# Kernel tuning notes

Hardware: AMD Instinct MI355X
Metric: run time of the kernel (lower is better)

## Reference

```python
import jax, jax.numpy as jnp
import numpy as np

B, S, H = 32, 4096, 512
N = 2 * H  # n = hidden_size * 2


def setup_inputs() -> dict:
    key = jax.random.key(0)
    ks = jax.random.split(key, 10)
    scale = 1.0 / np.sqrt(N)
    return {
        "dec_in_state": jax.random.normal(ks[0], (B, N), jnp.float32),
        "enc_states": jax.random.normal(ks[1], (B, S, N), jnp.float32),
        "enc_lens": jax.random.randint(ks[2], (B,), 1, S + 1),
        "coverage_vector": jax.random.uniform(ks[3], (B, S), jnp.float32),
        "Wh": jax.random.normal(ks[4], (N, N), jnp.float32) * scale,
        "bh": jnp.zeros((N,), jnp.float32),
        "Ws": jax.random.normal(ks[5], (N, N), jnp.float32) * scale,
        "bs": jnp.zeros((N,), jnp.float32),
        "wc": jax.random.normal(ks[6], (N,), jnp.float32) * scale,  # W_c: Linear(1, N, bias=False)
        "v": jax.random.normal(ks[7], (N,), jnp.float32) * scale,   # v: Linear(N, 1, bias=False)
    }


def reference(dec_in_state, enc_states, enc_lens, coverage_vector, Wh, bh, Ws, bs, wc, v):
    seq_len = enc_states.shape[1]
    # additive Bahdanau features: [B,S,N]
    enc_feats = jnp.einsum("bsn,mn->bsm", enc_states, Wh) + bh
    dec_feats = dec_in_state @ Ws.T + bs  # [B,N]
    cov_feats = coverage_vector[..., None] * wc  # [B,S,N] (Linear(1,N,no bias))
    e = jnp.tanh(enc_feats + dec_feats[:, None, :] + cov_feats) @ v  # [B,S]
    # masked renormalized softmax
    mask = (jnp.arange(seq_len)[None, :] < enc_lens[:, None]).astype(e.dtype)  # [B,S]
    attn = jax.nn.softmax(e, axis=1) * mask
    attn = attn / attn.sum(axis=1, keepdims=True)
    context = jnp.einsum("bs,bsn->bn", attn, enc_states)  # [B,N]
    coverage_out = coverage_vector + attn
    return (context, attn, coverage_out)
```

## Files before the change

kernel.cpp:

```cpp
#include <hip/hip_runtime.h>
#include <math.h>

#define B 32
#define S 4096
#define N 1024
#define L2E 1.4426950408889634f

typedef short short8 __attribute__((ext_vector_type(8)));
typedef short short4v __attribute__((ext_vector_type(4)));
typedef float float4v __attribute__((ext_vector_type(4)));

__device__ inline short f2bf(float f) {
    unsigned u = __builtin_bit_cast(unsigned, f);
    u += 0x7fffu + ((u >> 16) & 1u);
    return (short)(u >> 16);
}

__device__ __forceinline__ void load_lds16(const void* g, void* l) {
    __builtin_amdgcn_global_load_lds(
        (const __attribute__((address_space(1))) void*)g,
        (__attribute__((address_space(3))) void*)l, 16, 0, 0);
}

__global__ __launch_bounds__(256)
void prep_cvt_kernel(const float* __restrict__ dec, const float* __restrict__ Ws,
                     const float* __restrict__ bs, const float* __restrict__ enc,
                     const float* __restrict__ Wh, float* __restrict__ dec_feats,
                     float* __restrict__ e, short* __restrict__ encb,
                     short* __restrict__ whb) {
    unsigned bid = blockIdx.x;
    int tid = threadIdx.x;
    if (bid < 2048u) {
        if (bid < 512u) e[bid * 256 + tid] = 0.f;
        const size_t n8e = (size_t)B * S * N / 8;
        for (size_t i = (size_t)bid * 256 + tid; i < n8e; i += 2048u * 256u) {
            const float4v* s = (const float4v*)(enc + i * 8);
            float4v a = s[0], b = s[1];
            short8 o = { f2bf(a.x), f2bf(a.y), f2bf(a.z), f2bf(a.w),
                         f2bf(b.x), f2bf(b.y), f2bf(b.z), f2bf(b.w) };
            *(short8*)(encb + i * 8) = o;
        }
    } else if (bid < 2064u) {
        const size_t n8w = (size_t)N * N / 8;
        for (size_t i = (size_t)(bid - 2048u) * 256 + tid; i < n8w; i += 16u * 256u) {
            const float4v* s = (const float4v*)(Wh + i * 8);
            float4v a = s[0], b = s[1];
            short8 o = { f2bf(a.x), f2bf(a.y), f2bf(a.z), f2bf(a.w),
                         f2bf(b.x), f2bf(b.y), f2bf(b.z), f2bf(b.w) };
            *(short8*)(whb + i * 8) = o;
        }
    } else {
        int wid  = (int)(bid - 2064u) * 4 + (tid >> 6);
        int lane = tid & 63;
        int m = wid >> 5, b = wid & 31;
        const float4* drow = (const float4*)(dec + (size_t)b * N);
        const float4* wrow = (const float4*)(Ws + (size_t)m * N);
        float acc = 0.f;
#pragma unroll
        for (int k = 0; k < 4; ++k) {
            float4 a = drow[lane + (k << 6)];
            float4 w = wrow[lane + (k << 6)];
            acc += a.x * w.x + a.y * w.y + a.z * w.z + a.w * w.w;
        }
        acc += __shfl_xor(acc, 1);  acc += __shfl_xor(acc, 2);
        acc += __shfl_xor(acc, 4);  acc += __shfl_xor(acc, 8);
        acc += __shfl_xor(acc, 16); acc += __shfl_xor(acc, 32);
        if (lane == 0) dec_feats[(size_t)b * N + m] = acc + bs[m];
    }
}

__global__ __launch_bounds__(256)
void prep_kernel(const float* __restrict__ dec, const float* __restrict__ Ws,
                 const float* __restrict__ bs, float* __restrict__ dec_feats,
                 float* __restrict__ e) {
    int tg = blockIdx.x * 256 + threadIdx.x;
    if (tg < B * S) e[tg] = 0.f;
    int wid  = (blockIdx.x << 2) + (threadIdx.x >> 6);
    int lane = threadIdx.x & 63;
    int m = wid >> 5, b = wid & 31;
    const float4* drow = (const float4*)(dec + (size_t)b * N);
    const float4* wrow = (const float4*)(Ws + (size_t)m * N);
    float acc = 0.f;
#pragma unroll
    for (int k = 0; k < 4; ++k) {
        float4 a = drow[lane + (k << 6)];
        float4 w = wrow[lane + (k << 6)];
        acc += a.x * w.x + a.y * w.y + a.z * w.z + a.w * w.w;
    }
    acc += __shfl_xor(acc, 1);  acc += __shfl_xor(acc, 2);
    acc += __shfl_xor(acc, 4);  acc += __shfl_xor(acc, 8);
    acc += __shfl_xor(acc, 16); acc += __shfl_xor(acc, 32);
    if (lane == 0) dec_feats[(size_t)b * N + m] = acc + bs[m];
}

#define REGION_A(slot, hk) ((slot)*16384 + (hk)*8192)
#define REGION_B(slot, hk) (32768 + (slot)*16384 + (hk)*8192)

__global__ __launch_bounds__(512, 2)
void score_mfma8_kernel(const short* __restrict__ encb, const short* __restrict__ whb,
                        const float* __restrict__ bh, const float* __restrict__ dec_feats,
                        const float* __restrict__ cov, const float* __restrict__ wc,
                        const float* __restrict__ v, float* __restrict__ e) {
    __shared__ short lds[65536];

    unsigned bid = blockIdx.x;
    unsigned c = (bid & 7u) * 64u + (bid >> 3);
    int rtq = (int)(c >> 2), mtile = (int)(c & 3u);
    int m0 = mtile * 256;

    int t = threadIdx.x, lane = t & 63, w = t >> 6;
    int wm_ = w >> 2, wn_ = w & 3;
    int cq = lane >> 4, cm = lane & 15;

    int srow = lane >> 2;
    int sg = (lane & 3) ^ ((lane >> 3) & 3);
    const short* bS0 = whb + (size_t)(m0 + w * 16 + srow) * N + sg * 8;
    const short* bS1 = bS0 + (size_t)128 * N;
    const int dc0 = w * 512, dc1 = dc0 + 4096;

    int aoff[8], boff[4];
#pragma unroll
    for (int f = 0; f < 8; ++f) {
        int R = wm_ * 128 + f * 16 + cm;
        aoff[f] = R * 32 + ((cq ^ ((R >> 1) & 3)) << 3);
    }
#pragma unroll
    for (int j = 0; j < 4; ++j) {
        int R = wn_ * 64 + j * 16 + cm;
        boff[j] = R * 32 + ((cq ^ ((R >> 1) & 3)) << 3);
    }

    float basej[4], wcj[4], vj[4];
    {
        int bidx0 = rtq >> 2;
        const float* df = dec_feats + ((size_t)bidx0 << 10);
#pragma unroll
        for (int j = 0; j < 4; ++j) {
            int m = m0 + wn_ * 64 + j * 16 + cm;
            basej[j] = bh[m] + df[m];
            wcj[j]   = wc[m];
            vj[j]    = v[m];
        }
    }

#define STAGE(srcp0, srcp1, region, colElem) do {                         \
        int _cc = (colElem) & (N - 1);                                    \
        load_lds16((srcp0) + _cc, &lds[(region) + dc0]);                  \
        load_lds16((srcp1) + _cc, &lds[(region) + dc1]);                  \
    } while (0)

#define PHASE(slot, sub, SRC0, SRC1, SREGION, SCOL) do {                      \
        const int hk_ = (sub) >> 1, mh_ = (sub) & 1;                          \
        if (mh_ == 0) {                                                       \
            _Pragma("unroll")                                                 \
            for (int j = 0; j < 4; ++j)                                       \
                bf[j] = *(const short8*)&lds[REGION_B(slot, hk_) + boff[j]];  \
        }                                                                     \
        short8 af[4];                                                         \
        _Pragma("unroll")                                                     \
        for (int f = 0; f < 4; ++f)                                           \
            af[f] = *(const short8*)&lds[REGION_A(slot, hk_) + aoff[mh_ * 4 + f]]; \
        STAGE(SRC0, SRC1, SREGION, SCOL);                                     \
        __builtin_amdgcn_s_barrier();                                         \
        asm volatile("s_waitcnt lgkmcnt(0)" ::: "memory");                    \
        __builtin_amdgcn_sched_barrier(0);                                    \
        __builtin_amdgcn_s_setprio(1);                                        \
        _Pragma("unroll")                                                     \
        for (int f = 0; f < 4; ++f)                                           \
            _Pragma("unroll")                                                 \
            for (int j = 0; j < 4; ++j)                                       \
                acc[mh_ * 4 + f][j] = __builtin_amdgcn_mfma_f32_16x16x32_bf16(\
                    af[f], bf[j], acc[mh_ * 4 + f][j], 0, 0, 0);              \
        __builtin_amdgcn_s_setprio(0);                                        \
        if (mh_ == 1) asm volatile("s_waitcnt vmcnt(8)" ::: "memory");        \
        __builtin_amdgcn_s_barrier();                                         \
    } while (0)

#pragma unroll 1
    for (int it = 0; it < 4; ++it) {
        int r0 = (rtq * 4 + it) * 256;
        const short* aS0 = encb + (size_t)(r0 + w * 16 + srow) * N + sg * 8;
        const short* aS1 = aS0 + (size_t)128 * N;

        float4v acc[8][4];
#pragma unroll
        for (int f = 0; f < 8; ++f)
#pragma unroll
            for (int j = 0; j < 4; ++j) acc[f][j] = (float4v){0.f, 0.f, 0.f, 0.f};

        STAGE(aS0, aS1, REGION_A(0, 0), 0);
        STAGE(bS0, bS1, REGION_B(0, 0), 0);
        STAGE(aS0, aS1, REGION_A(0, 1), 32);
        STAGE(bS0, bS1, REGION_B(0, 1), 32);
        STAGE(aS0, aS1, REGION_A(1, 0), 64);
        STAGE(bS0, bS1, REGION_B(1, 0), 64);
        asm volatile("s_waitcnt vmcnt(8)" ::: "memory");
        __builtin_amdgcn_s_barrier();

        short8 bf[4];

#pragma unroll 1
        for (int i = 0; i < 8; ++i) {
            int kb = i * 128;
            PHASE(0, 0, aS0, aS1, REGION_A(1, 1), kb + 96);
            PHASE(0, 1, bS0, bS1, REGION_B(1, 1), kb + 96);
            PHASE(0, 2, aS0, aS1, REGION_A(0, 0), kb + 128);
            PHASE(0, 3, bS0, bS1, REGION_B(0, 0), kb + 128);
            PHASE(1, 0, aS0, aS1, REGION_A(0, 1), kb + 160);
            PHASE(1, 1, bS0, bS1, REGION_B(0, 1), kb + 160);
            PHASE(1, 2, aS0, aS1, REGION_A(1, 0), kb + 192);
            PHASE(1, 3, bS0, bS1, REGION_B(1, 0), kb + 192);
        }
        asm volatile("s_waitcnt vmcnt(0)" ::: "memory");

#pragma unroll
        for (int f = 0; f < 8; ++f) {
            int rbase = r0 + wm_ * 128 + f * 16 + cq * 4;
            float4v cvv = *(const float4v*)&cov[rbase];
            float cv[4] = {cvv.x, cvv.y, cvv.z, cvv.w};
            float rs[4] = {0.f, 0.f, 0.f, 0.f};
#pragma unroll
            for (int j = 0; j < 4; ++j) {
#pragma unroll
                for (int reg = 0; reg < 4; ++reg) {
                    float val = acc[f][j][reg] + basej[j] + cv[reg] * wcj[j];
                    val = fminf(fmaxf(val, -15.f), 15.f);
                    float t2 = __builtin_amdgcn_exp2f(val * 2.8853900817779268f);
                    float r  = __builtin_amdgcn_rcpf(t2 + 1.f);
                    float th = fmaf(-2.f, r, 1.f);
                    rs[reg] = fmaf(th, vj[j], rs[reg]);
                }
            }
#pragma unroll
            for (int reg = 0; reg < 4; ++reg) {
                float p = rs[reg];
                p += __shfl_xor(p, 1);
                p += __shfl_xor(p, 2);
                p += __shfl_xor(p, 4);
                p += __shfl_xor(p, 8);
                if (cm == 0) atomicAdd(&e[rbase + reg], p);
            }
        }
        asm volatile("s_waitcnt vmcnt(0)" ::: "memory");
        __builtin_amdgcn_s_barrier();
    }
#undef PHASE
#undef STAGE
}

#define BR 128
#define BM 128
#define BK 64
#define LDK (BK + 8)

__global__ __launch_bounds__(256)
void score_mfma_kernel(const float* __restrict__ enc, const float* __restrict__ Wh,
                       const float* __restrict__ bh, const float* __restrict__ dec_feats,
                       const float* __restrict__ cov, const float* __restrict__ wc,
                       const float* __restrict__ v, float* __restrict__ e) {
    __shared__ short As[BR][LDK];
    __shared__ short Bs[BM][LDK];

    unsigned h   = blockIdx.x;
    unsigned xcd = h & 7u;
    unsigned mt  = (h >> 3) & 7u;
    unsigned g   = h >> 6;
    int r0 = (int)(xcd + 8u * g) * BR;
    int m0 = (int)mt * BM;

    int t    = threadIdx.x;
    int lane = t & 63;
    int w    = t >> 6;
    int wr   = (w >> 1) * 64;
    int wm   = (w & 1) * 64;
    int cq   = lane >> 4;
    int cm   = lane & 15;

    float4v acc[4][4];
#pragma unroll
    for (int i = 0; i < 4; ++i)
#pragma unroll
        for (int j = 0; j < 4; ++j) acc[i][j] = (float4v){0.f, 0.f, 0.f, 0.f};

    int srow = t >> 4;
    int scol = (t & 15) * 4;

    for (int k0 = 0; k0 < N; k0 += BK) {
#pragma unroll
        for (int p = 0; p < 8; ++p) {
            int row = p * 16 + srow;
            float4v a = *(const float4v*)(enc + (size_t)(r0 + row) * N + k0 + scol);
            short4v ap = { f2bf(a.x), f2bf(a.y), f2bf(a.z), f2bf(a.w) };
            *(short4v*)&As[row][scol] = ap;
            float4v bq = *(const float4v*)(Wh + (size_t)(m0 + row) * N + k0 + scol);
            short4v bp = { f2bf(bq.x), f2bf(bq.y), f2bf(bq.z), f2bf(bq.w) };
            *(short4v*)&Bs[row][scol] = bp;
        }
        __syncthreads();
#pragma unroll
        for (int ks = 0; ks < BK; ks += 32) {
            short8 af[4], bfr[4];
#pragma unroll
            for (int i = 0; i < 4; ++i)
                af[i] = *(const short8*)&As[wr + i * 16 + cm][ks + cq * 8];
#pragma unroll
            for (int j = 0; j < 4; ++j)
                bfr[j] = *(const short8*)&Bs[wm + j * 16 + cm][ks + cq * 8];
#pragma unroll
            for (int i = 0; i < 4; ++i)
#pragma unroll
                for (int j = 0; j < 4; ++j)
                    acc[i][j] = __builtin_amdgcn_mfma_f32_16x16x32_bf16(
                        af[i], bfr[j], acc[i][j], 0, 0, 0);
        }
        __syncthreads();
    }

    int b = r0 >> 12;
    const float* df = dec_feats + ((size_t)b << 10);

    float basej[4], wcj[4], vj[4];
#pragma unroll
    for (int j = 0; j < 4; ++j) {
        int m = m0 + wm + j * 16 + cm;
        basej[j] = bh[m] + df[m];
        wcj[j]   = wc[m];
        vj[j]    = v[m];
    }

#pragma unroll
    for (int i = 0; i < 4; ++i) {
        int rbase = r0 + wr + i * 16 + cq * 4;
        float cv[4];
#pragma unroll
        for (int reg = 0; reg < 4; ++reg) cv[reg] = cov[rbase + reg];
        float rs[4] = {0.f, 0.f, 0.f, 0.f};
#pragma unroll
        for (int j = 0; j < 4; ++j) {
#pragma unroll
            for (int reg = 0; reg < 4; ++reg) {
                float val = acc[i][j][reg] + basej[j] + cv[reg] * wcj[j];
                val = fminf(fmaxf(val, -15.f), 15.f);
                float t2 = __builtin_amdgcn_exp2f(val * 2.8853900817779268f);
                float r  = __builtin_amdgcn_rcpf(t2 + 1.f);
                float th = fmaf(-2.f, r, 1.f);
                rs[reg] = fmaf(th, vj[j], rs[reg]);
            }
        }
#pragma unroll
        for (int reg = 0; reg < 4; ++reg) {
            float p = rs[reg];
            p += __shfl_xor(p, 1);
            p += __shfl_xor(p, 2);
            p += __shfl_xor(p, 4);
            p += __shfl_xor(p, 8);
            if (cm == 0) atomicAdd(&e[rbase + reg], p);
        }
    }
}

__global__ __launch_bounds__(256)
void softmax_partial_kernel(const float* __restrict__ e, const int* __restrict__ lens,
                            float2* __restrict__ pm) {
    int b = blockIdx.y, ch = blockIdx.x;
    int t = threadIdx.x, lane = t & 63, wid = t >> 6;
    int len = lens[b];
    int s0 = ch * 512;
    const float* eb = e + (size_t)b * S + s0;
    float v0 = (s0 + t       < len) ? eb[t]       : -INFINITY;
    float v1 = (s0 + t + 256 < len) ? eb[t + 256] : -INFINITY;
    float mx = fmaxf(v0, v1);
    mx = fmaxf(mx, __shfl_xor(mx, 1));  mx = fmaxf(mx, __shfl_xor(mx, 2));
    mx = fmaxf(mx, __shfl_xor(mx, 4));  mx = fmaxf(mx, __shfl_xor(mx, 8));
    mx = fmaxf(mx, __shfl_xor(mx, 16)); mx = fmaxf(mx, __shfl_xor(mx, 32));
    __shared__ float redm[4], reds[4];
    if (lane == 0) redm[wid] = mx;
    __syncthreads();
    mx = fmaxf(fmaxf(redm[0], redm[1]), fmaxf(redm[2], redm[3]));

    float sum = 0.f;
    if (mx > -INFINITY)
        sum = exp2f((v0 - mx) * L2E) + exp2f((v1 - mx) * L2E);
    sum += __shfl_xor(sum, 1);  sum += __shfl_xor(sum, 2);
    sum += __shfl_xor(sum, 4);  sum += __shfl_xor(sum, 8);
    sum += __shfl_xor(sum, 16); sum += __shfl_xor(sum, 32);
    if (lane == 0) reds[wid] = sum;
    __syncthreads();
    if (t == 0) {
        float2 p; p.x = mx; p.y = reds[0] + reds[1] + reds[2] + reds[3];
        pm[b * 8 + ch] = p;
    }
}

#define SCH 64
__global__ __launch_bounds__(256)
void context_part_kernel(const float* __restrict__ e, const int* __restrict__ lens,
                         const float2* __restrict__ pm, const float* __restrict__ cov,
                         const float* __restrict__ enc, float* __restrict__ attn,
                         float* __restrict__ cov_out, float* __restrict__ part) {
    int b  = blockIdx.y;
    int ch = blockIdx.x;
    int s0 = ch * (S / SCH);
    int tid = threadIdx.x;
    __shared__ float a_lds[S / SCH];

    if (tid < S / SCH) {
        int len = lens[b];
        const float2* pb = pm + b * 8;
        float M = -INFINITY;
#pragma unroll
        for (int i = 0; i < 8; ++i) M = fmaxf(M, pb[i].x);
        float Ssum = 0.f;
#pragma unroll
        for (int i = 0; i < 8; ++i)
            Ssum += pb[i].y * exp2f((pb[i].x - M) * L2E);
        float inv = 1.f / Ssum;
        int s = s0 + tid;
        float ew = e[(size_t)b * S + s];
        float a = (s < len) ? exp2f((ew - M) * L2E) * inv : 0.f;
        a_lds[tid] = a;
        attn[(size_t)b * S + s] = a;
        cov_out[(size_t)b * S + s] = cov[(size_t)b * S + s] + a;
    }
    __syncthreads();

    const float4* ep = (const float4*)(enc + ((size_t)b * S + s0) * N);
    float4 acc = {0.f, 0.f, 0.f, 0.f};
    for (int s = 0; s < S / SCH; ++s) {
        float a = a_lds[s];
        float4 ev = ep[(size_t)s * (N / 4) + tid];
        acc.x += a * ev.x; acc.y += a * ev.y;
        acc.z += a * ev.z; acc.w += a * ev.w;
    }
    *(float4*)&part[((size_t)b * SCH + ch) * N + tid * 4] = acc;
}

__global__ __launch_bounds__(256)
void context_reduce_kernel(const float* __restrict__ part, float* __restrict__ ctx) {
    int idx = blockIdx.x * 256 + threadIdx.x;
    int b = idx >> 10, n = idx & (N - 1);
    const float* p = part + (size_t)b * SCH * N + n;
    float acc = 0.f;
#pragma unroll
    for (int c2 = 0; c2 < SCH; ++c2) acc += p[(size_t)c2 * N];
    ctx[idx] = acc;
}

__global__ __launch_bounds__(1024)
void softmax_kernel(const float* __restrict__ e, const int* __restrict__ lens,
                    const float* __restrict__ cov,
                    float* __restrict__ attn, float* __restrict__ cov_out) {
    int b = blockIdx.x, t = threadIdx.x;
    int lane = t & 63, wid = t >> 6;
    int len = lens[b];
    const float* eb = e + (size_t)b * S;
    __shared__ float redm[16], reds[16];

    float ev[4];
    float mx = -INFINITY;
#pragma unroll
    for (int k = 0; k < 4; ++k) {
        int s = t + (k << 10);
        ev[k] = (s < len) ? eb[s] : -INFINITY;
        mx = fmaxf(mx, ev[k]);
    }
    mx = fmaxf(mx, __shfl_xor(mx, 1));  mx = fmaxf(mx, __shfl_xor(mx, 2));
    mx = fmaxf(mx, __shfl_xor(mx, 4));  mx = fmaxf(mx, __shfl_xor(mx, 8));
    mx = fmaxf(mx, __shfl_xor(mx, 16)); mx = fmaxf(mx, __shfl_xor(mx, 32));
    if (lane == 0) redm[wid] = mx;
    __syncthreads();
    if (t < 16) {
        float v2 = redm[t];
        v2 = fmaxf(v2, __shfl_xor(v2, 1)); v2 = fmaxf(v2, __shfl_xor(v2, 2));
        v2 = fmaxf(v2, __shfl_xor(v2, 4)); v2 = fmaxf(v2, __shfl_xor(v2, 8));
        if (t == 0) redm[0] = v2;
    }
    __syncthreads();
    mx = redm[0];

    float ex[4];
    float sum = 0.f;
#pragma unroll
    for (int k = 0; k < 4; ++k) {
        int s = t + (k << 10);
        ex[k] = exp2f((ev[k] - mx) * L2E);
        sum += ex[k];
    }
    sum += __shfl_xor(sum, 1);  sum += __shfl_xor(sum, 2);
    sum += __shfl_xor(sum, 4);  sum += __shfl_xor(sum, 8);
    sum += __shfl_xor(sum, 16); sum += __shfl_xor(sum, 32);
    if (lane == 0) reds[wid] = sum;
    __syncthreads();
    if (t < 16) {
        float v2 = reds[t];
        v2 += __shfl_xor(v2, 1); v2 += __shfl_xor(v2, 2);
        v2 += __shfl_xor(v2, 4); v2 += __shfl_xor(v2, 8);
        if (t == 0) reds[0] = v2;
    }
    __syncthreads();
    float inv = 1.f / reds[0];

#pragma unroll
    for (int k = 0; k < 4; ++k) {
        int s = t + (k << 10);
        float a = ex[k] * inv;
        attn[(size_t)b * S + s] = a;
        cov_out[(size_t)b * S + s] = cov[(size_t)b * S + s] + a;
    }
}

__global__ __launch_bounds__(256)
void context_kernel(const float* __restrict__ attn, const float* __restrict__ enc,
                    float* __restrict__ ctx) {
    int b  = blockIdx.y;
    int s0 = blockIdx.x * (S / SCH);
    int n4 = threadIdx.x;
    const float4* ep = (const float4*)(enc + ((size_t)b * S + s0) * N);
    float4 acc = {0.f, 0.f, 0.f, 0.f};
    for (int s = 0; s < S / SCH; ++s) {
        float a = attn[(size_t)b * S + s0 + s];
        float4 ev = ep[(size_t)s * (N / 4) + n4];
        acc.x += a * ev.x; acc.y += a * ev.y;
        acc.z += a * ev.z; acc.w += a * ev.w;
    }
    float* cp = ctx + (size_t)b * N + n4 * 4;
    atomicAdd(cp + 0, acc.x);
    atomicAdd(cp + 1, acc.y);
    atomicAdd(cp + 2, acc.z);
    atomicAdd(cp + 3, acc.w);
}

extern "C" void kernel_launch(void* const* d_in, const int* in_sizes, int n_in,
                              void* d_out, int out_size, void* d_ws, size_t ws_size,
                              hipStream_t stream) {
    const float* dec  = (const float*)d_in[0];
    const float* enc  = (const float*)d_in[1];
    const int*   lens = (const int*)  d_in[2];
    const float* cov  = (const float*)d_in[3];
    const float* Wh   = (const float*)d_in[4];
    const float* bh   = (const float*)d_in[5];
    const float* Ws   = (const float*)d_in[6];
    const float* bs   = (const float*)d_in[7];
    const float* wc   = (const float*)d_in[8];
    const float* v    = (const float*)d_in[9];

    float* out     = (float*)d_out;
    float* ctx     = out;
    float* attn    = out + (size_t)B * N;
    float* cov_out = attn + (size_t)B * S;

    size_t off_e    = (size_t)B * N * 4;
    size_t off_encb = off_e + (size_t)B * S * 4;
    size_t off_whb  = off_encb + (size_t)B * S * N * 2;
    size_t off_part = off_whb + (size_t)N * N * 2;
    size_t off_pm   = off_part + (size_t)B * SCH * N * 4;
    size_t need     = off_pm + (size_t)B * 8 * sizeof(float2);

    float* dec_feats = (float*)d_ws;
    float* e         = (float*)((char*)d_ws + off_e);

    if (ws_size >= need) {
        short*  encb = (short*)((char*)d_ws + off_encb);
        short*  whb  = (short*)((char*)d_ws + off_whb);
        float*  part = (float*)((char*)d_ws + off_part);
        float2* pm   = (float2*)((char*)d_ws + off_pm);
        prep_cvt_kernel<<<10256, 256, 0, stream>>>(dec, Ws, bs, enc, Wh,
                                                   dec_feats, e, encb, whb);
        score_mfma8_kernel<<<512, 512, 0, stream>>>(
            encb, whb, bh, dec_feats, cov, wc, v, e);
        softmax_partial_kernel<<<dim3(8, B), 256, 0, stream>>>(e, lens, pm);
        context_part_kernel<<<dim3(SCH, B), 256, 0, stream>>>(
            e, lens, pm, cov, enc, attn, cov_out, part);
        context_reduce_kernel<<<(B * N) / 256, 256, 0, stream>>>(part, ctx);
    } else {
        prep_kernel<<<8192, 256, 0, stream>>>(dec, Ws, bs, dec_feats, e);
        hipMemsetAsync(ctx, 0, (size_t)B * N * sizeof(float), stream);
        score_mfma_kernel<<<(B * S / BR) * (N / BM), 256, 0, stream>>>(
            enc, Wh, bh, dec_feats, cov, wc, v, e);
        softmax_kernel<<<B, 1024, 0, stream>>>(e, lens, cov, attn, cov_out);
        context_kernel<<<dim3(SCH, B), 256, 0, stream>>>(attn, enc, ctx);
    }
}
```

Before: 1.165 ms.

## Give each score block a full row tile across all M tiles, drop atomics

The score kernel now assigns each block one 256-row tile of encoder states and loops over all four 256-column tiles of Wh, instead of a row group over one column tile. The encoder A tile is reused from LDS across column tiles, tanh·v partial sums stay in registers, and a final LDS reduction writes e directly. This removes the global atomicAdds and the zeroing of e in the prep kernel. The trade-off is a 32-entry per-thread accumulator that raises register pressure, so launch bounds drop to one block per SM. The restaging between column tiles also waits on vmcnt(0), which serialises loads.

```diff
diff --git a/kernel.cpp b/kernel.cpp
--- a/kernel.cpp
+++ b/kernel.cpp
@@ -26,12 +26,10 @@
 void prep_cvt_kernel(const float* __restrict__ dec, const float* __restrict__ Ws,
                      const float* __restrict__ bs, const float* __restrict__ enc,
                      const float* __restrict__ Wh, float* __restrict__ dec_feats,
-                     float* __restrict__ e, short* __restrict__ encb,
-                     short* __restrict__ whb) {
+                     short* __restrict__ encb, short* __restrict__ whb) {
     unsigned bid = blockIdx.x;
     int tid = threadIdx.x;
     if (bid < 2048u) {
-        if (bid < 512u) e[bid * 256 + tid] = 0.f;
         const size_t n8e = (size_t)B * S * N / 8;
         for (size_t i = (size_t)bid * 256 + tid; i < n8e; i += 2048u * 256u) {
             const float4v* s = (const float4v*)(enc + i * 8);
@@ -96,7 +94,7 @@
 #define REGION_A(slot, hk) ((slot)*16384 + (hk)*8192)
 #define REGION_B(slot, hk) (32768 + (slot)*16384 + (hk)*8192)
 
-__global__ __launch_bounds__(512, 2)
+__global__ __launch_bounds__(512, 1)
 void score_mfma8_kernel(const short* __restrict__ encb, const short* __restrict__ whb,
                         const float* __restrict__ bh, const float* __restrict__ dec_feats,
                         const float* __restrict__ cov, const float* __restrict__ wc,
@@ -105,8 +103,8 @@
 
     unsigned bid = blockIdx.x;
     unsigned c = (bid & 7u) * 64u + (bid >> 3);
-    int rtq = (int)(c >> 2), mtile = (int)(c & 3u);
-    int m0 = mtile * 256;
+    int rt = (int)c;
+    int r0 = rt * 256;
 
     int t = threadIdx.x, lane = t & 63, w = t >> 6;
     int wm_ = w >> 2, wn_ = w & 3;
@@ -114,8 +112,8 @@
 
     int srow = lane >> 2;
     int sg = (lane & 3) ^ ((lane >> 3) & 3);
-    const short* bS0 = whb + (size_t)(m0 + w * 16 + srow) * N + sg * 8;
-    const short* bS1 = bS0 + (size_t)128 * N;
+    const short* aS0 = encb + (size_t)(r0 + w * 16 + srow) * N + sg * 8;
+    const short* aS1 = aS0 + (size_t)128 * N;
     const int dc0 = w * 512, dc1 = dc0 + 4096;
 
     int aoff[8], boff[4];
@@ -130,18 +128,14 @@
         boff[j] = R * 32 + ((cq ^ ((R >> 1) & 3)) << 3);
     }
 
-    float basej[4], wcj[4], vj[4];
-    {
-        int bidx0 = rtq >> 2;
-        const float* df = dec_feats + ((size_t)bidx0 << 10);
-#pragma unroll
-        for (int j = 0; j < 4; ++j) {
-            int m = m0 + wn_ * 64 + j * 16 + cm;
-            basej[j] = bh[m] + df[m];
-            wcj[j]   = wc[m];
-            vj[j]    = v[m];
-        }
-    }
+    int bidx = r0 >> 12;
+    const float* df = dec_feats + ((size_t)bidx << 10);
+
+    float rs[8][4];
+#pragma unroll
+    for (int f = 0; f < 8; ++f)
+#pragma unroll
+        for (int reg = 0; reg < 4; ++reg) rs[f][reg] = 0.f;
 
 #define STAGE(srcp0, srcp1, region, colElem) do {                         \
         int _cc = (colElem) & (N - 1);                                    \
@@ -177,10 +171,10 @@
     } while (0)
 
 #pragma unroll 1
-    for (int it = 0; it < 4; ++it) {
-        int r0 = (rtq * 4 + it) * 256;
-        const short* aS0 = encb + (size_t)(r0 + w * 16 + srow) * N + sg * 8;
-        const short* aS1 = aS0 + (size_t)128 * N;
+    for (int mt = 0; mt < 4; ++mt) {
+        int m0 = mt * 256;
+        const short* bS0 = whb + (size_t)(m0 + w * 16 + srow) * N + sg * 8;
+        const short* bS1 = bS0 + (size_t)128 * N;
 
         float4v acc[8][4];
 #pragma unroll
@@ -188,14 +182,23 @@
 #pragma unroll
             for (int j = 0; j < 4; ++j) acc[f][j] = (float4v){0.f, 0.f, 0.f, 0.f};
 
-        STAGE(aS0, aS1, REGION_A(0, 0), 0);
-        STAGE(bS0, bS1, REGION_B(0, 0), 0);
-        STAGE(aS0, aS1, REGION_A(0, 1), 32);
-        STAGE(bS0, bS1, REGION_B(0, 1), 32);
-        STAGE(aS0, aS1, REGION_A(1, 0), 64);
-        STAGE(bS0, bS1, REGION_B(1, 0), 64);
-        asm volatile("s_waitcnt vmcnt(8)" ::: "memory");
-        __builtin_amdgcn_s_barrier();
+        if (mt == 0) {
+            STAGE(aS0, aS1, REGION_A(0, 0), 0);
+            STAGE(bS0, bS1, REGION_B(0, 0), 0);
+            STAGE(aS0, aS1, REGION_A(0, 1), 32);
+            STAGE(bS0, bS1, REGION_B(0, 1), 32);
+            STAGE(aS0, aS1, REGION_A(1, 0), 64);
+            STAGE(bS0, bS1, REGION_B(1, 0), 64);
+            asm volatile("s_waitcnt vmcnt(8)" ::: "memory");
+            __builtin_amdgcn_s_barrier();
+        } else {
+            asm volatile("s_waitcnt vmcnt(0)" ::: "memory");
+            STAGE(bS0, bS1, REGION_B(0, 0), 0);
+            STAGE(bS0, bS1, REGION_B(0, 1), 32);
+            STAGE(bS0, bS1, REGION_B(1, 0), 64);
+            asm volatile("s_waitcnt vmcnt(0)" ::: "memory");
+            __builtin_amdgcn_s_barrier();
+        }
 
         short8 bf[4];
 
@@ -211,14 +214,20 @@
             PHASE(1, 2, aS0, aS1, REGION_A(1, 0), kb + 192);
             PHASE(1, 3, bS0, bS1, REGION_B(1, 0), kb + 192);
         }
-        asm volatile("s_waitcnt vmcnt(0)" ::: "memory");
-
+
+        float basej[4], wcj[4], vj[4];
+#pragma unroll
+        for (int j = 0; j < 4; ++j) {
+            int m = m0 + wn_ * 64 + j * 16 + cm;
+            basej[j] = bh[m] + df[m];
+            wcj[j]   = wc[m];
+            vj[j]    = v[m];
+        }
 #pragma unroll
         for (int f = 0; f < 8; ++f) {
             int rbase = r0 + wm_ * 128 + f * 16 + cq * 4;
             float4v cvv = *(const float4v*)&cov[rbase];
             float cv[4] = {cvv.x, cvv.y, cvv.z, cvv.w};
-            float rs[4] = {0.f, 0.f, 0.f, 0.f};
 #pragma unroll
             for (int j = 0; j < 4; ++j) {
 #pragma unroll
@@ -228,24 +237,35 @@
                     float t2 = __builtin_amdgcn_exp2f(val * 2.8853900817779268f);
                     float r  = __builtin_amdgcn_rcpf(t2 + 1.f);
                     float th = fmaf(-2.f, r, 1.f);
-                    rs[reg] = fmaf(th, vj[j], rs[reg]);
+                    rs[f][reg] = fmaf(th, vj[j], rs[f][reg]);
                 }
             }
-#pragma unroll
-            for (int reg = 0; reg < 4; ++reg) {
-                float p = rs[reg];
-                p += __shfl_xor(p, 1);
-                p += __shfl_xor(p, 2);
-                p += __shfl_xor(p, 4);
-                p += __shfl_xor(p, 8);
-                if (cm == 0) atomicAdd(&e[rbase + reg], p);
-            }
-        }
-        asm volatile("s_waitcnt vmcnt(0)" ::: "memory");
-        __builtin_amdgcn_s_barrier();
+        }
     }
 #undef PHASE
 #undef STAGE
+
+    asm volatile("s_waitcnt vmcnt(0)" ::: "memory");
+    __builtin_amdgcn_s_barrier();
+    float* red = (float*)lds;
+#pragma unroll
+    for (int f = 0; f < 8; ++f) {
+#pragma unroll
+        for (int reg = 0; reg < 4; ++reg) {
+            float p = rs[f][reg];
+            p += __shfl_xor(p, 1);
+            p += __shfl_xor(p, 2);
+            p += __shfl_xor(p, 4);
+            p += __shfl_xor(p, 8);
+            if (cm == 0)
+                red[wn_ * 256 + wm_ * 128 + f * 16 + cq * 4 + reg] = p;
+        }
+    }
+    __syncthreads();
+    if (t < 256) {
+        float ev = red[t] + red[256 + t] + red[512 + t] + red[768 + t];
+        e[r0 + t] = ev;
+    }
 }
 
 #define BR 128
@@ -334,7 +354,7 @@
         float cv[4];
 #pragma unroll
         for (int reg = 0; reg < 4; ++reg) cv[reg] = cov[rbase + reg];
-        float rs[4] = {0.f, 0.f, 0.f, 0.f};
+        float rsl[4] = {0.f, 0.f, 0.f, 0.f};
 #pragma unroll
         for (int j = 0; j < 4; ++j) {
 #pragma unroll
@@ -344,12 +364,12 @@
                 float t2 = __builtin_amdgcn_exp2f(val * 2.8853900817779268f);
                 float r  = __builtin_amdgcn_rcpf(t2 + 1.f);
                 float th = fmaf(-2.f, r, 1.f);
-                rs[reg] = fmaf(th, vj[j], rs[reg]);
+                rsl[reg] = fmaf(th, vj[j], rsl[reg]);
             }
         }
 #pragma unroll
         for (int reg = 0; reg < 4; ++reg) {
-            float p = rs[reg];
+            float p = rsl[reg];
             p += __shfl_xor(p, 1);
             p += __shfl_xor(p, 2);
             p += __shfl_xor(p, 4);
@@ -482,7 +502,6 @@
     float sum = 0.f;
 #pragma unroll
     for (int k = 0; k < 4; ++k) {
-        int s = t + (k << 10);
         ex[k] = exp2f((ev[k] - mx) * L2E);
         sum += ex[k];
     }
@@ -565,7 +584,7 @@
         float*  part = (float*)((char*)d_ws + off_part);
         float2* pm   = (float2*)((char*)d_ws + off_pm);
         prep_cvt_kernel<<<10256, 256, 0, stream>>>(dec, Ws, bs, enc, Wh,
-                                                   dec_feats, e, encb, whb);
+                                                   dec_feats, encb, whb);
         score_mfma8_kernel<<<512, 512, 0, stream>>>(
             encb, whb, bh, dec_feats, cov, wc, v, e);
         softmax_partial_kernel<<<dim3(8, B), 256, 0, stream>>>(e, lens, pm);
```

After: 1.124 ms. 1.04x faster.
